# Optimization experiments

Measured on AMD Instinct MI355X. Metric: run time of the kernel, lower is better.

Reference implementation:

```python
import jax, jax.numpy as jnp
import numpy as np

N_HEADS = 4
DIM_K = 64
DIM_V = 64
D_MODEL = 256


def setup_inputs() -> dict:
    key = jax.random.key(0)
    ks = jax.random.split(key, 10)
    B, S = 8, 1024
    s = 1.0 / np.sqrt(D_MODEL)
    return {
        "x": jax.random.normal(ks[0], (B, S, D_MODEL), jnp.float32),
        "y": jax.random.normal(ks[1], (B, S, D_MODEL), jnp.float32),
        "Wq": jax.random.normal(ks[2], (D_MODEL, DIM_K * N_HEADS), jnp.float32) * s,
        "bq": jnp.zeros((DIM_K * N_HEADS,), jnp.float32),
        "Wk": jax.random.normal(ks[3], (D_MODEL, DIM_K * N_HEADS), jnp.float32) * s,
        "bk": jnp.zeros((DIM_K * N_HEADS,), jnp.float32),
        "Wv": jax.random.normal(ks[4], (D_MODEL, DIM_V * N_HEADS), jnp.float32) * s,
        "bv": jnp.zeros((DIM_V * N_HEADS,), jnp.float32),
        "Wo": jax.random.normal(ks[5], (DIM_V * N_HEADS, D_MODEL), jnp.float32) * s,
        "bo": jnp.zeros((D_MODEL,), jnp.float32),
    }


def reference(x, y, Wq, bq, Wk, bk, Wv, bv, Wo, bo):
    B, Sx, _ = x.shape
    Sy = y.shape[1]
    dk = DIM_K // N_HEADS  # head dim for Q/K (16)
    dv = DIM_V // N_HEADS  # head dim for V (16)
    # Faithful to the original reshape: leading dim becomes n_heads^2 pseudo-heads.
    Q = (x @ Wq + bq).reshape(-1, B, Sx, dk)   # [H2, B, Sx, dk]
    K = (y @ Wk + bk).reshape(-1, B, Sy, dk)   # [H2, B, Sy, dk]
    V = (y @ Wv + bv).reshape(-1, B, Sy, dv)   # [H2, B, Sy, dv]
    scale = 1.0 / np.sqrt(DIM_K)
    scores = jnp.einsum("hbqd,hbkd->hbqk", Q, K) * scale  # [H2, B, Sx, Sy]
    # Per-row lower median (torch.median semantics: lower of two middle values).
    n = scores.shape[-1]
    med = jnp.sort(scores, axis=-1)[..., (n - 1) // 2][..., None]
    # Mask out entries not strictly greater than the row median.
    scores = jnp.where(scores - med > 0, scores, -jnp.inf)
    probs = jax.nn.softmax(scores, axis=-1)
    out = jnp.einsum("hbqk,hbkd->hbqd", probs, V)          # [H2, B, Sx, dv]
    out = jnp.transpose(out, (0, 2, 1, 3)).reshape(B, Sx, -1)  # [B, Sx, H2*dv]
    return out @ Wo + bo
```

## Files before the change

### kernel.cpp

```cpp
#include <hip/hip_runtime.h>
#include <stdint.h>


typedef _Float16 f16x8 __attribute__((ext_vector_type(8)));
typedef _Float16 f16x4 __attribute__((ext_vector_type(4)));
typedef _Float16 f16x2 __attribute__((ext_vector_type(2)));
typedef float    f32x4 __attribute__((ext_vector_type(4)));

__device__ __forceinline__ void gemm_mfma(const float* __restrict__ A,
                                          const float* __restrict__ W,
                                          const float* __restrict__ bias,
                                          float* __restrict__ C)
{
    __shared__ _Float16 Bhi[64][136];
    __shared__ _Float16 Blo[64][136];
    const int tid = threadIdx.x;
    const int m0 = blockIdx.x << 6, n0 = blockIdx.y << 6;

    const int wv = tid >> 6, lane = tid & 63;
    const int fm = lane & 15, fq = lane >> 4;
    const int arow = m0 + (wv << 4) + fm;

    f32x4 acc[4];
    #pragma unroll
    for (int cb = 0; cb < 4; ++cb) { acc[cb][0]=0.f; acc[cb][1]=0.f; acc[cb][2]=0.f; acc[cb][3]=0.f; }

    #pragma unroll
    for (int h = 0; h < 2; ++h) {
        if (h) __syncthreads();
        {
            const int kk = (tid & 63) << 1;
            const int nh = (tid >> 6) << 4;
            const float* w0 = W + (size_t)((h << 7) + kk) * 256 + n0 + nh;
            const float* w1 = w0 + 256;
            #pragma unroll
            for (int c4 = 0; c4 < 4; ++c4) {
                float4 v0 = *(const float4*)(w0 + (c4 << 2));
                float4 v1 = *(const float4*)(w1 + (c4 << 2));
                const float e0[4] = {v0.x, v0.y, v0.z, v0.w};
                const float e1[4] = {v1.x, v1.y, v1.z, v1.w};
                #pragma unroll
                for (int jj = 0; jj < 4; ++jj) {
                    const int n = nh + (c4 << 2) + jj;
                    _Float16 h0 = (_Float16)e0[jj];
                    _Float16 h1 = (_Float16)e1[jj];
                    f16x2 hp; hp[0] = h0; hp[1] = h1;
                    f16x2 lp; lp[0] = (_Float16)(e0[jj] - (float)h0);
                              lp[1] = (_Float16)(e1[jj] - (float)h1);
                    *(f16x2*)&Bhi[n][kk] = hp;
                    *(f16x2*)&Blo[n][kk] = lp;
                }
            }
        }
        __syncthreads();

        #pragma unroll
        for (int kb = 0; kb < 4; ++kb) {
            const float* ap = A + (size_t)arow * 256 + (h << 7) + (kb << 5) + (fq << 3);
            float4 a0 = *(const float4*)ap;
            float4 a1 = *(const float4*)(ap + 4);
            const float ae[8] = {a0.x, a0.y, a0.z, a0.w, a1.x, a1.y, a1.z, a1.w};
            f16x8 Ah, Al;
            #pragma unroll
            for (int j = 0; j < 8; ++j) {
                _Float16 hh = (_Float16)ae[j];
                Ah[j] = hh;
                Al[j] = (_Float16)(ae[j] - (float)hh);
            }
            #pragma unroll
            for (int cb = 0; cb < 4; ++cb) {
                f16x8 Bh = *(const f16x8*)&Bhi[(cb << 4) + fm][(kb << 5) + (fq << 3)];
                f16x8 Bl = *(const f16x8*)&Blo[(cb << 4) + fm][(kb << 5) + (fq << 3)];
                acc[cb] = __builtin_amdgcn_mfma_f32_16x16x32_f16(Ah, Bh, acc[cb], 0, 0, 0);
                acc[cb] = __builtin_amdgcn_mfma_f32_16x16x32_f16(Al, Bh, acc[cb], 0, 0, 0);
                acc[cb] = __builtin_amdgcn_mfma_f32_16x16x32_f16(Ah, Bl, acc[cb], 0, 0, 0);
            }
        }
    }

    #pragma unroll
    for (int cb = 0; cb < 4; ++cb) {
        const float bb = bias[n0 + (cb << 4) + fm];
        #pragma unroll
        for (int i = 0; i < 4; ++i)
            C[(size_t)(m0 + (wv << 4) + (fq << 2) + i) * 256
              + n0 + (cb << 4) + fm] = acc[cb][i] + bb;
    }
}

__global__ __attribute__((amdgpu_waves_per_eu(4, 4)))
__launch_bounds__(256) void gemmQKV(
    const float* __restrict__ x, const float* __restrict__ y,
    const float* __restrict__ Wq, const float* __restrict__ bq,
    const float* __restrict__ Wk, const float* __restrict__ bk,
    const float* __restrict__ Wv, const float* __restrict__ bv,
    float* __restrict__ Q, float* __restrict__ K, float* __restrict__ V)
{
    const int z = blockIdx.z;
    const float* A = (z == 0) ? x  : y;
    const float* W = (z == 0) ? Wq : (z == 1) ? Wk : Wv;
    const float* b = (z == 0) ? bq : (z == 1) ? bk : bv;
    float*       C = (z == 0) ? Q  : (z == 1) ? K  : V;
    gemm_mfma(A, W, b, C);
}

__global__ __attribute__((amdgpu_waves_per_eu(4, 4)))
__launch_bounds__(256) void gemmOut(
    const float* __restrict__ A, const float* __restrict__ W,
    const float* __restrict__ b, float* __restrict__ C)
{
    gemm_mfma(A, W, b, C);
}

__device__ __forceinline__ float u2f(unsigned int m) {
    unsigned int x = (m & 0x80000000u) ? (m ^ 0x80000000u) : ~m;
    return __uint_as_float(x);
}
__device__ __forceinline__ unsigned int f2u(float f) {
    unsigned int x = __float_as_uint(f);
    return (x & 0x80000000u) ? ~x : (x | 0x80000000u);
}

__device__ __forceinline__ float wred_sum(float x) {
    x += __int_as_float(__builtin_amdgcn_update_dpp(0, __float_as_int(x), 0x111, 0xF, 0xF, true));
    x += __int_as_float(__builtin_amdgcn_update_dpp(0, __float_as_int(x), 0x112, 0xF, 0xF, true));
    x += __int_as_float(__builtin_amdgcn_update_dpp(0, __float_as_int(x), 0x114, 0xF, 0xF, true));
    x += __int_as_float(__builtin_amdgcn_update_dpp(0, __float_as_int(x), 0x118, 0xF, 0xF, true));
    x += __int_as_float(__builtin_amdgcn_update_dpp(0, __float_as_int(x), 0x142, 0xF, 0xF, true));
    x += __int_as_float(__builtin_amdgcn_update_dpp(0, __float_as_int(x), 0x143, 0xF, 0xF, true));
    return __int_as_float(__builtin_amdgcn_readlane(__float_as_int(x), 63));
}
__device__ __forceinline__ float wred_min(float x) {
    const int IDENT = 0x7f7fffff;
    x = fminf(x, __int_as_float(__builtin_amdgcn_update_dpp(IDENT, __float_as_int(x), 0x111, 0xF, 0xF, false)));
    x = fminf(x, __int_as_float(__builtin_amdgcn_update_dpp(IDENT, __float_as_int(x), 0x112, 0xF, 0xF, false)));
    x = fminf(x, __int_as_float(__builtin_amdgcn_update_dpp(IDENT, __float_as_int(x), 0x114, 0xF, 0xF, false)));
    x = fminf(x, __int_as_float(__builtin_amdgcn_update_dpp(IDENT, __float_as_int(x), 0x118, 0xF, 0xF, false)));
    x = fminf(x, __int_as_float(__builtin_amdgcn_update_dpp(IDENT, __float_as_int(x), 0x142, 0xF, 0xF, false)));
    x = fminf(x, __int_as_float(__builtin_amdgcn_update_dpp(IDENT, __float_as_int(x), 0x143, 0xF, 0xF, false)));
    return __int_as_float(__builtin_amdgcn_readlane(__float_as_int(x), 63));
}
__device__ __forceinline__ float wred_max(float x) {
    const int IDENT = (int)0xff7fffff;
    x = fmaxf(x, __int_as_float(__builtin_amdgcn_update_dpp(IDENT, __float_as_int(x), 0x111, 0xF, 0xF, false)));
    x = fmaxf(x, __int_as_float(__builtin_amdgcn_update_dpp(IDENT, __float_as_int(x), 0x112, 0xF, 0xF, false)));
    x = fmaxf(x, __int_as_float(__builtin_amdgcn_update_dpp(IDENT, __float_as_int(x), 0x114, 0xF, 0xF, false)));
    x = fmaxf(x, __int_as_float(__builtin_amdgcn_update_dpp(IDENT, __float_as_int(x), 0x118, 0xF, 0xF, false)));
    x = fmaxf(x, __int_as_float(__builtin_amdgcn_update_dpp(IDENT, __float_as_int(x), 0x142, 0xF, 0xF, false)));
    x = fmaxf(x, __int_as_float(__builtin_amdgcn_update_dpp(IDENT, __float_as_int(x), 0x143, 0xF, 0xF, false)));
    return __int_as_float(__builtin_amdgcn_readlane(__float_as_int(x), 63));
}

__global__ __attribute__((amdgpu_waves_per_eu(6, 6)))
__launch_bounds__(512) void attn(
    const float* __restrict__ Qb, const float* __restrict__ Kb,
    const float* __restrict__ Vb, float* __restrict__ Ob)
{
    __shared__ union {
        float    Ssc[8][1028];
        _Float16 Vt[16][1032];
    } U;
    __shared__ float part[1024];
    __shared__ float sums[2][8];

    const int tid  = threadIdx.x;
    const int wave = tid >> 6, lane = tid & 63;
    const int head = blockIdx.x, grp = blockIdx.y;
    const float* Qh = Qb + ((size_t)head << 14);
    const float* Kh = Kb + ((size_t)head << 14);
    const float* Vh = Vb + ((size_t)head << 14);
    const int fm = lane & 15, fq = lane >> 4;

    for (int i = tid; i < 4096; i += 512) {
        float4 v = ((const float4*)Vh)[i];
        const int k = i >> 2, d0 = (i & 3) << 2;
        U.Vt[d0 + 0][k] = (_Float16)v.x;
        U.Vt[d0 + 1][k] = (_Float16)v.y;
        U.Vt[d0 + 2][k] = (_Float16)v.z;
        U.Vt[d0 + 3][k] = (_Float16)v.w;
    }
    __syncthreads();
    f16x8 Vf[4];
    #pragma unroll
    for (int kb = 0; kb < 4; ++kb)
        Vf[kb] = *(const f16x8*)&U.Vt[fm][(((wave << 2) + kb) << 5) + (fq << 3)];

    f16x8 Bp[8];
    #pragma unroll
    for (int kb = 0; kb < 8; ++kb) {
        const int krow = (wave << 7) + (kb << 4) + fm;
        float4 kv = *(const float4*)(Kh + ((size_t)krow << 4) + (fq << 2));
        const float ke[4] = {kv.x * 0.125f, kv.y * 0.125f,
                             kv.z * 0.125f, kv.w * 0.125f};
        #pragma unroll
        for (int j = 0; j < 4; ++j) {
            _Float16 h = (_Float16)ke[j];
            Bp[kb][j]     = h;
            Bp[kb][j + 4] = (_Float16)(ke[j] - (float)h);
        }
    }
    __syncthreads();

    const int cstart = (grp * 128) / 6;
    const int cend   = ((grp + 1) * 128) / 6;

    for (int chunk = cstart; chunk < cend; ++chunk) {
        const int qbase = chunk << 3;
        const int sb = chunk & 1;

        f16x8 A1, A2;
        {
            const int arow = qbase + (fm & 7);
            float4 qv = *(const float4*)(Qh + ((size_t)arow << 4) + (fq << 2));
            const float qe[4] = {qv.x, qv.y, qv.z, qv.w};
            #pragma unroll
            for (int j = 0; j < 4; ++j) {
                _Float16 h = (_Float16)qe[j];
                A1[j] = h; A1[j + 4] = h;
                A2[j] = (_Float16)(qe[j] - (float)h);
                A2[j + 4] = (_Float16)0.f;
            }
        }
        #pragma unroll
        for (int kb = 0; kb < 8; ++kb) {
            f32x4 c = {0.f, 0.f, 0.f, 0.f};
            c = __builtin_amdgcn_mfma_f32_16x16x32_f16(A1, Bp[kb], c, 0, 0, 0);
            c = __builtin_amdgcn_mfma_f32_16x16x32_f16(A2, Bp[kb], c, 0, 0, 0);
            if (fq < 2) {
                const int col = (wave << 7) + (kb << 4) + fm;
                #pragma unroll
                for (int i = 0; i < 4; ++i)
                    U.Ssc[(fq << 2) + i][col] = c[i];
            }
        }
        __syncthreads();

        float s[16];
        #pragma unroll
        for (int b = 0; b < 4; ++b) {
            f32x4 v = *(const f32x4*)&U.Ssc[wave][(b << 8) + (lane << 2)];
            s[(b << 2) + 0] = v.x; s[(b << 2) + 1] = v.y;
            s[(b << 2) + 2] = v.z; s[(b << 2) + 3] = v.w;
        }

        float mn = 0.f, sq = 0.f;
        #pragma unroll
        for (int j = 0; j < 16; ++j) { mn += s[j]; sq += s[j] * s[j]; }
        mn = wred_sum(mn);
        sq = wred_sum(sq);
        mn *= (1.0f / 1024.0f);
        const float var  = fmaxf(sq * (1.0f / 1024.0f) - mn * mn, 1e-12f);
        const float step = __builtin_sqrtf(var) * 0.0024479f;

        unsigned int lo = 0x00800000u, hi = 0xFF7FFFFFu;
        int cl = 0, ch = 1024;
        float vL = -3.4e38f, vH = 3.4e38f;
        float t = mn, medf = 0.f;
        int found = 0;
        for (int pass = 0; pass < 64 && !found; ++pass) {
            int cnt = 0;
            #pragma unroll
            for (int j = 0; j < 16; ++j)
                cnt += __popcll(__ballot(s[j] <= t));
            const unsigned int tc = f2u(t);
            if (cnt >= 512) { hi = tc; ch = cnt; vH = t; }
            else            { lo = tc + 1; cl = cnt; vL = t; }

            if (cl == 511) {
                float c = 3.4e38f;
                #pragma unroll
                for (int j = 0; j < 16; ++j)
                    c = fminf(c, (s[j] > vL) ? s[j] : 3.4e38f);
                medf = wred_min(c); found = 1;
            } else if (ch == 512) {
                float c = -3.4e38f;
                #pragma unroll
                for (int j = 0; j < 16; ++j)
                    c = fmaxf(c, (s[j] <= vH) ? s[j] : -3.4e38f);
                medf = wred_max(c); found = 1;
            } else if (cl == 510) {
                float m1 = 3.4e38f;
                #pragma unroll
                for (int j = 0; j < 16; ++j)
                    m1 = fminf(m1, (s[j] > vL) ? s[j] : 3.4e38f);
                m1 = wred_min(m1);
                int c1 = 0;
                #pragma unroll
                for (int j = 0; j < 16; ++j)
                    c1 += __popcll(__ballot(s[j] <= m1));
                if (c1 >= 512) { medf = m1; }
                else {
                    float c2 = 3.4e38f;
                    #pragma unroll
                    for (int j = 0; j < 16; ++j)
                        c2 = fminf(c2, (s[j] > m1) ? s[j] : 3.4e38f);
                    medf = wred_min(c2);
                }
                found = 1;
            } else if (ch == 513) {
                float m1 = -3.4e38f;
                #pragma unroll
                for (int j = 0; j < 16; ++j)
                    m1 = fmaxf(m1, (s[j] <= vH) ? s[j] : -3.4e38f);
                m1 = wred_max(m1);
                int c1 = 0;
                #pragma unroll
                for (int j = 0; j < 16; ++j)
                    c1 += __popcll(__ballot(s[j] < m1));
                if (c1 <= 511) { medf = m1; }
                else {
                    float c2 = -3.4e38f;
                    #pragma unroll
                    for (int j = 0; j < 16; ++j)
                        c2 = fmaxf(c2, (s[j] < m1) ? s[j] : -3.4e38f);
                    medf = wred_max(c2);
                }
                found = 1;
            } else if (lo >= hi) {
                medf = u2f(lo); found = 1;
            } else {
                float tn = t + (511.5f - (float)cnt) * step;
                bool ok = (tn > vL) && (tn < vH);
                if (pass >= 5 && (pass & 1)) ok = false;
                t = ok ? tn : u2f(lo + ((hi - lo) >> 1));
            }
        }
        if (!found) medf = u2f(lo);

        _Float16* Pw = (_Float16*)&U.Ssc[wave][0];
        float sum = 0.f;
        #pragma unroll
        for (int b = 0; b < 4; ++b) {
            f16x4 hv;
            #pragma unroll
            for (int jj = 0; jj < 4; ++jj) {
                float e = (s[(b << 2) + jj] > medf) ? __expf(s[(b << 2) + jj]) : 0.f;
                _Float16 h = (_Float16)e;
                hv[jj] = h;
                sum += (float)h;
            }
            *(f16x4*)&Pw[(b << 8) + (lane << 2)] = hv;
        }
        sum = wred_sum(sum);
        if (lane == 0) sums[sb][wave] = sum;
        __syncthreads();

        f32x4 acc = {0.f, 0.f, 0.f, 0.f};
        const _Float16* Pr = (const _Float16*)&U.Ssc[fm & 7][0] + (fq << 3);
        #pragma unroll
        for (int kb = 0; kb < 4; ++kb) {
            f16x8 a = *(const f16x8*)(Pr + ((((wave << 2) + kb)) << 5));
            acc = __builtin_amdgcn_mfma_f32_16x16x32_f16(a, Vf[kb], acc, 0, 0, 0);
        }
        if (lane < 32) {
            #pragma unroll
            for (int i = 0; i < 4; ++i)
                part[(wave << 7) + (((fq << 2) + i) << 4) + fm] = acc[i];
        }
        __syncthreads();

        const int rw = (wave - chunk) & 7;
        if (rw < 2) {
            const int t2 = (rw << 6) + lane;
            const int r = t2 >> 4, d = t2 & 15;
            float o = 0.f;
            #pragma unroll
            for (int w = 0; w < 8; ++w) o += part[(w << 7) + t2];
            const float inv = 1.0f / sums[sb][r];
            const int q = qbase + r;
            const int h = head >> 3, bp = head & 7;
            float* dst = Ob + (((size_t)(h >> 1)) << 18)
                            + ((size_t)(((h & 1) << 9) + (q >> 1)) << 8)
                            + ((q & 1) << 7) + (bp << 4) + d;
            *dst = o * inv;
        }
    }
}

extern "C" void kernel_launch(void* const* d_in, const int* in_sizes, int n_in,
                              void* d_out, int out_size, void* d_ws, size_t ws_size,
                              hipStream_t stream) {
    const float* x  = (const float*)d_in[0];
    const float* y  = (const float*)d_in[1];
    const float* Wq = (const float*)d_in[2];
    const float* bq = (const float*)d_in[3];
    const float* Wk = (const float*)d_in[4];
    const float* bk = (const float*)d_in[5];
    const float* Wv = (const float*)d_in[6];
    const float* bv = (const float*)d_in[7];
    const float* Wo = (const float*)d_in[8];
    const float* bo = (const float*)d_in[9];
    float* out = (float*)d_out;

    float* Q  = (float*)d_ws;
    float* K  = Q + 2097152;
    float* V  = K + 2097152;
    float* AO = V + 2097152;

    gemmQKV<<<dim3(128, 4, 3), dim3(256), 0, stream>>>(x, y, Wq, bq, Wk, bk,
                                                       Wv, bv, Q, K, V);
    attn<<<dim3(128, 6), dim3(512), 0, stream>>>(Q, K, V, AO);
    gemmOut<<<dim3(128, 4), dim3(256), 0, stream>>>(AO, Wo, bo, out);
}
```

Before: 285.1 us.

## Use secant-based median search and prefetch A/Q operands one step ahead

Changes the median search to a secant step built from the previous threshold and count, falling back to the fixed step otherwise, and delays the forced bisection from pass 5 to pass 8. The goal is fewer ballot-count passes per row. Also prefetches the next A tile in the projection GEMM and the next Q row in the attention loop so load latency overlaps compute, and splits the min/max reductions into two accumulators to shorten dependency chains. The prefetches keep extra values live in registers, and the secant step could take more passes on some rows.

```diff
diff --git a/kernel.cpp b/kernel.cpp
--- a/kernel.cpp
+++ b/kernel.cpp
@@ -20,10 +20,14 @@
     const int wv = tid >> 6, lane = tid & 63;
     const int fm = lane & 15, fq = lane >> 4;
     const int arow = m0 + (wv << 4) + fm;
+    const float* abase = A + (size_t)arow * 256;
 
     f32x4 acc[4];
     #pragma unroll
     for (int cb = 0; cb < 4; ++cb) { acc[cb][0]=0.f; acc[cb][1]=0.f; acc[cb][2]=0.f; acc[cb][3]=0.f; }
+
+    float4 a0 = *(const float4*)(abase + (fq << 3));
+    float4 a1 = *(const float4*)(abase + (fq << 3) + 4);
 
     #pragma unroll
     for (int h = 0; h < 2; ++h) {
@@ -56,9 +60,13 @@
 
         #pragma unroll
         for (int kb = 0; kb < 4; ++kb) {
-            const float* ap = A + (size_t)arow * 256 + (h << 7) + (kb << 5) + (fq << 3);
-            float4 a0 = *(const float4*)ap;
-            float4 a1 = *(const float4*)(ap + 4);
+            const int ks = (h << 2) + kb;
+            float4 n0v = a0, n1v = a1;
+            if (ks < 7) {
+                const float* np = abase + ((ks + 1) << 5) + (fq << 3);
+                n0v = *(const float4*)np;
+                n1v = *(const float4*)(np + 4);
+            }
             const float ae[8] = {a0.x, a0.y, a0.z, a0.w, a1.x, a1.y, a1.z, a1.w};
             f16x8 Ah, Al;
             #pragma unroll
@@ -75,6 +83,7 @@
                 acc[cb] = __builtin_amdgcn_mfma_f32_16x16x32_f16(Al, Bh, acc[cb], 0, 0, 0);
                 acc[cb] = __builtin_amdgcn_mfma_f32_16x16x32_f16(Ah, Bl, acc[cb], 0, 0, 0);
             }
+            a0 = n0v; a1 = n1v;
         }
     }
 
@@ -204,14 +213,18 @@
     const int cstart = (grp * 128) / 6;
     const int cend   = ((grp + 1) * 128) / 6;
 
+    float4 qv;
+    {
+        const int arow0 = (cstart << 3) + (fm & 7);
+        qv = *(const float4*)(Qh + ((size_t)arow0 << 4) + (fq << 2));
+    }
+
     for (int chunk = cstart; chunk < cend; ++chunk) {
         const int qbase = chunk << 3;
         const int sb = chunk & 1;
 
         f16x8 A1, A2;
         {
-            const int arow = qbase + (fm & 7);
-            float4 qv = *(const float4*)(Qh + ((size_t)arow << 4) + (fq << 2));
             const float qe[4] = {qv.x, qv.y, qv.z, qv.w};
             #pragma unroll
             for (int j = 0; j < 4; ++j) {
@@ -220,6 +233,10 @@
                 A2[j] = (_Float16)(qe[j] - (float)h);
                 A2[j + 4] = (_Float16)0.f;
             }
+        }
+        if (chunk + 1 < cend) {
+            const int arow = ((chunk + 1) << 3) + (fm & 7);
+            qv = *(const float4*)(Qh + ((size_t)arow << 4) + (fq << 2));
         }
         #pragma unroll
         for (int kb = 0; kb < 8; ++kb) {
@@ -256,6 +273,7 @@
         int cl = 0, ch = 1024;
         float vL = -3.4e38f, vH = 3.4e38f;
         float t = mn, medf = 0.f;
+        float tp = 0.f; int cp = -1;
         int found = 0;
         for (int pass = 0; pass < 64 && !found; ++pass) {
             int cnt = 0;
@@ -267,61 +285,83 @@
             else            { lo = tc + 1; cl = cnt; vL = t; }
 
             if (cl == 511) {
-                float c = 3.4e38f;
-                #pragma unroll
-                for (int j = 0; j < 16; ++j)
-                    c = fminf(c, (s[j] > vL) ? s[j] : 3.4e38f);
-                medf = wred_min(c); found = 1;
+                float c0 = 3.4e38f, c1 = 3.4e38f;
+                #pragma unroll
+                for (int j = 0; j < 8; ++j) {
+                    c0 = fminf(c0, (s[j]     > vL) ? s[j]     : 3.4e38f);
+                    c1 = fminf(c1, (s[j + 8] > vL) ? s[j + 8] : 3.4e38f);
+                }
+                medf = wred_min(fminf(c0, c1)); found = 1;
             } else if (ch == 512) {
-                float c = -3.4e38f;
-                #pragma unroll
-                for (int j = 0; j < 16; ++j)
-                    c = fmaxf(c, (s[j] <= vH) ? s[j] : -3.4e38f);
-                medf = wred_max(c); found = 1;
+                float c0 = -3.4e38f, c1 = -3.4e38f;
+                #pragma unroll
+                for (int j = 0; j < 8; ++j) {
+                    c0 = fmaxf(c0, (s[j]     <= vH) ? s[j]     : -3.4e38f);
+                    c1 = fmaxf(c1, (s[j + 8] <= vH) ? s[j + 8] : -3.4e38f);
+                }
+                medf = wred_max(fmaxf(c0, c1)); found = 1;
             } else if (cl == 510) {
-                float m1 = 3.4e38f;
-                #pragma unroll
-                for (int j = 0; j < 16; ++j)
-                    m1 = fminf(m1, (s[j] > vL) ? s[j] : 3.4e38f);
-                m1 = wred_min(m1);
+                float m0 = 3.4e38f, m1 = 3.4e38f;
+                #pragma unroll
+                for (int j = 0; j < 8; ++j) {
+                    m0 = fminf(m0, (s[j]     > vL) ? s[j]     : 3.4e38f);
+                    m1 = fminf(m1, (s[j + 8] > vL) ? s[j + 8] : 3.4e38f);
+                }
+                m1 = wred_min(fminf(m0, m1));
                 int c1 = 0;
                 #pragma unroll
                 for (int j = 0; j < 16; ++j)
                     c1 += __popcll(__ballot(s[j] <= m1));
                 if (c1 >= 512) { medf = m1; }
                 else {
-                    float c2 = 3.4e38f;
+                    float d0 = 3.4e38f, d1 = 3.4e38f;
                     #pragma unroll
-                    for (int j = 0; j < 16; ++j)
-                        c2 = fminf(c2, (s[j] > m1) ? s[j] : 3.4e38f);
-                    medf = wred_min(c2);
+                    for (int j = 0; j < 8; ++j) {
+                        d0 = fminf(d0, (s[j]     > m1) ? s[j]     : 3.4e38f);
+                        d1 = fminf(d1, (s[j + 8] > m1) ? s[j + 8] : 3.4e38f);
+                    }
+                    medf = wred_min(fminf(d0, d1));
                 }
                 found = 1;
             } else if (ch == 513) {
-                float m1 = -3.4e38f;
-                #pragma unroll
-                for (int j = 0; j < 16; ++j)
-                    m1 = fmaxf(m1, (s[j] <= vH) ? s[j] : -3.4e38f);
-                m1 = wred_max(m1);
+                float m0 = -3.4e38f, m1 = -3.4e38f;
+                #pragma unroll
+                for (int j = 0; j < 8; ++j) {
+                    m0 = fmaxf(m0, (s[j]     <= vH) ? s[j]     : -3.4e38f);
+                    m1 = fmaxf(m1, (s[j + 8] <= vH) ? s[j + 8] : -3.4e38f);
+                }
+                m1 = wred_max(fmaxf(m0, m1));
                 int c1 = 0;
                 #pragma unroll
                 for (int j = 0; j < 16; ++j)
                     c1 += __popcll(__ballot(s[j] < m1));
                 if (c1 <= 511) { medf = m1; }
                 else {
-                    float c2 = -3.4e38f;
+                    float d0 = -3.4e38f, d1 = -3.4e38f;
                     #pragma unroll
-                    for (int j = 0; j < 16; ++j)
-                        c2 = fmaxf(c2, (s[j] < m1) ? s[j] : -3.4e38f);
-                    medf = wred_max(c2);
+                    for (int j = 0; j < 8; ++j) {
+                        d0 = fmaxf(d0, (s[j]     < m1) ? s[j]     : -3.4e38f);
+                        d1 = fmaxf(d1, (s[j + 8] < m1) ? s[j + 8] : -3.4e38f);
+                    }
+                    medf = wred_max(fmaxf(d0, d1));
                 }
                 found = 1;
             } else if (lo >= hi) {
                 medf = u2f(lo); found = 1;
             } else {
-                float tn = t + (511.5f - (float)cnt) * step;
+                float tn;
+                bool have = false;
+                if (cp >= 0 && cnt != cp) {
+                    const float slope = (t - tp) / (float)(cnt - cp);
+                    if (slope > 0.f) {
+                        tn = t + (511.5f - (float)cnt) * slope;
+                        have = true;
+                    }
+                }
+                if (!have) tn = t + (511.5f - (float)cnt) * step;
+                tp = t; cp = cnt;
                 bool ok = (tn > vL) && (tn < vH);
-                if (pass >= 5 && (pass & 1)) ok = false;
+                if (pass >= 8 && (pass & 1)) ok = false;
                 t = ok ? tn : u2f(lo + ((hi - lo) >> 1));
             }
         }
```

Measured after the change: 305.7 us. 7.2% more time.

## Pre-split weights into fp16 hi/lo once and store V as fp16

Applied to the files above, without the earlier changes.

Adds a prepW kernel that transposes each weight matrix and splits it into fp16 high and low parts a single time. The GEMMs then read these directly from global memory instead of converting the fp32 weights in every block through LDS with syncthreads. The QKV GEMM also writes V as fp16, which halves V traffic and removes the conversion in the attention kernel. The cost is one extra kernel launch, more workspace, and GEMM B-operand reads that now come from global or L2 without LDS staging.

```diff
diff --git a/kernel.cpp b/kernel.cpp
--- a/kernel.cpp
+++ b/kernel.cpp
@@ -4,112 +4,128 @@
 
 typedef _Float16 f16x8 __attribute__((ext_vector_type(8)));
 typedef _Float16 f16x4 __attribute__((ext_vector_type(4)));
-typedef _Float16 f16x2 __attribute__((ext_vector_type(2)));
 typedef float    f32x4 __attribute__((ext_vector_type(4)));
 
+__global__ __launch_bounds__(256) void prepW(
+    const float* __restrict__ Wq, const float* __restrict__ Wk,
+    const float* __restrict__ Wv, const float* __restrict__ Wo,
+    _Float16* __restrict__ P)
+{
+    __shared__ float T[64][65];
+    const int mat = blockIdx.y;
+    const float* W = (mat == 0) ? Wq : (mat == 1) ? Wk : (mat == 2) ? Wv : Wo;
+    const int tk = blockIdx.x >> 2, tn = blockIdx.x & 3;
+    const int t  = threadIdx.x;
+    const int cl = t & 63, rg = t >> 6;
+
+    #pragma unroll
+    for (int r = 0; r < 16; ++r) {
+        const int k = (rg << 4) + r;
+        T[k][cl] = W[(size_t)((tk << 6) + k) * 256 + (tn << 6) + cl];
+    }
+    __syncthreads();
+    _Float16* hi = P + ((size_t)mat << 17);
+    _Float16* lo = hi + 65536;
+    #pragma unroll
+    for (int r = 0; r < 16; ++r) {
+        const int n = (rg << 4) + r;
+        const float v = T[cl][n];
+        const _Float16 h = (_Float16)v;
+        const size_t o = (size_t)((tn << 6) + n) * 256 + (tk << 6) + cl;
+        hi[o] = h;
+        lo[o] = (_Float16)(v - (float)h);
+    }
+}
+
 __device__ __forceinline__ void gemm_mfma(const float* __restrict__ A,
-                                          const float* __restrict__ W,
+                                          const _Float16* __restrict__ Whi,
+                                          const _Float16* __restrict__ Wlo,
                                           const float* __restrict__ bias,
-                                          float* __restrict__ C)
+                                          float* __restrict__ C, int vf16)
 {
-    __shared__ _Float16 Bhi[64][136];
-    __shared__ _Float16 Blo[64][136];
     const int tid = threadIdx.x;
     const int m0 = blockIdx.x << 6, n0 = blockIdx.y << 6;
-
     const int wv = tid >> 6, lane = tid & 63;
     const int fm = lane & 15, fq = lane >> 4;
     const int arow = m0 + (wv << 4) + fm;
+    const float*     abase = A   + (size_t)arow * 256 + (fq << 3);
+    const _Float16*  bh0   = Whi + (size_t)(n0 + fm) * 256 + (fq << 3);
+    const _Float16*  bl0   = Wlo + (size_t)(n0 + fm) * 256 + (fq << 3);
 
     f32x4 acc[4];
     #pragma unroll
     for (int cb = 0; cb < 4; ++cb) { acc[cb][0]=0.f; acc[cb][1]=0.f; acc[cb][2]=0.f; acc[cb][3]=0.f; }
 
-    #pragma unroll
-    for (int h = 0; h < 2; ++h) {
-        if (h) __syncthreads();
-        {
-            const int kk = (tid & 63) << 1;
-            const int nh = (tid >> 6) << 4;
-            const float* w0 = W + (size_t)((h << 7) + kk) * 256 + n0 + nh;
-            const float* w1 = w0 + 256;
-            #pragma unroll
-            for (int c4 = 0; c4 < 4; ++c4) {
-                float4 v0 = *(const float4*)(w0 + (c4 << 2));
-                float4 v1 = *(const float4*)(w1 + (c4 << 2));
-                const float e0[4] = {v0.x, v0.y, v0.z, v0.w};
-                const float e1[4] = {v1.x, v1.y, v1.z, v1.w};
-                #pragma unroll
-                for (int jj = 0; jj < 4; ++jj) {
-                    const int n = nh + (c4 << 2) + jj;
-                    _Float16 h0 = (_Float16)e0[jj];
-                    _Float16 h1 = (_Float16)e1[jj];
-                    f16x2 hp; hp[0] = h0; hp[1] = h1;
-                    f16x2 lp; lp[0] = (_Float16)(e0[jj] - (float)h0);
-                              lp[1] = (_Float16)(e1[jj] - (float)h1);
-                    *(f16x2*)&Bhi[n][kk] = hp;
-                    *(f16x2*)&Blo[n][kk] = lp;
-                }
-            }
-        }
-        __syncthreads();
-
-        #pragma unroll
-        for (int kb = 0; kb < 4; ++kb) {
-            const float* ap = A + (size_t)arow * 256 + (h << 7) + (kb << 5) + (fq << 3);
-            float4 a0 = *(const float4*)ap;
-            float4 a1 = *(const float4*)(ap + 4);
-            const float ae[8] = {a0.x, a0.y, a0.z, a0.w, a1.x, a1.y, a1.z, a1.w};
-            f16x8 Ah, Al;
-            #pragma unroll
-            for (int j = 0; j < 8; ++j) {
-                _Float16 hh = (_Float16)ae[j];
-                Ah[j] = hh;
-                Al[j] = (_Float16)(ae[j] - (float)hh);
-            }
-            #pragma unroll
-            for (int cb = 0; cb < 4; ++cb) {
-                f16x8 Bh = *(const f16x8*)&Bhi[(cb << 4) + fm][(kb << 5) + (fq << 3)];
-                f16x8 Bl = *(const f16x8*)&Blo[(cb << 4) + fm][(kb << 5) + (fq << 3)];
-                acc[cb] = __builtin_amdgcn_mfma_f32_16x16x32_f16(Ah, Bh, acc[cb], 0, 0, 0);
-                acc[cb] = __builtin_amdgcn_mfma_f32_16x16x32_f16(Al, Bh, acc[cb], 0, 0, 0);
-                acc[cb] = __builtin_amdgcn_mfma_f32_16x16x32_f16(Ah, Bl, acc[cb], 0, 0, 0);
-            }
-        }
-    }
-
-    #pragma unroll
-    for (int cb = 0; cb < 4; ++cb) {
-        const float bb = bias[n0 + (cb << 4) + fm];
-        #pragma unroll
-        for (int i = 0; i < 4; ++i)
-            C[(size_t)(m0 + (wv << 4) + (fq << 2) + i) * 256
-              + n0 + (cb << 4) + fm] = acc[cb][i] + bb;
+    #pragma unroll 2
+    for (int ks = 0; ks < 8; ++ks) {
+        float4 a0 = *(const float4*)(abase + (ks << 5));
+        float4 a1 = *(const float4*)(abase + (ks << 5) + 4);
+        const float ae[8] = {a0.x, a0.y, a0.z, a0.w, a1.x, a1.y, a1.z, a1.w};
+        f16x8 Ah, Al;
+        #pragma unroll
+        for (int j = 0; j < 8; ++j) {
+            const _Float16 hh = (_Float16)ae[j];
+            Ah[j] = hh;
+            Al[j] = (_Float16)(ae[j] - (float)hh);
+        }
+        #pragma unroll
+        for (int cb = 0; cb < 4; ++cb) {
+            const size_t off = ((size_t)(cb << 4) << 8) + (ks << 5);
+            f16x8 Bh = *(const f16x8*)(bh0 + off);
+            f16x8 Bl = *(const f16x8*)(bl0 + off);
+            acc[cb] = __builtin_amdgcn_mfma_f32_16x16x32_f16(Ah, Bh, acc[cb], 0, 0, 0);
+            acc[cb] = __builtin_amdgcn_mfma_f32_16x16x32_f16(Al, Bh, acc[cb], 0, 0, 0);
+            acc[cb] = __builtin_amdgcn_mfma_f32_16x16x32_f16(Ah, Bl, acc[cb], 0, 0, 0);
+        }
+    }
+
+    if (vf16) {
+        _Float16* Cv = (_Float16*)C;
+        #pragma unroll
+        for (int cb = 0; cb < 4; ++cb) {
+            const float bb = bias[n0 + (cb << 4) + fm];
+            #pragma unroll
+            for (int i = 0; i < 4; ++i)
+                Cv[(size_t)(m0 + (wv << 4) + (fq << 2) + i) * 256
+                   + n0 + (cb << 4) + fm] = (_Float16)(acc[cb][i] + bb);
+        }
+    } else {
+        #pragma unroll
+        for (int cb = 0; cb < 4; ++cb) {
+            const float bb = bias[n0 + (cb << 4) + fm];
+            #pragma unroll
+            for (int i = 0; i < 4; ++i)
+                C[(size_t)(m0 + (wv << 4) + (fq << 2) + i) * 256
+                  + n0 + (cb << 4) + fm] = acc[cb][i] + bb;
+        }
     }
 }
 
 __global__ __attribute__((amdgpu_waves_per_eu(4, 4)))
 __launch_bounds__(256) void gemmQKV(
     const float* __restrict__ x, const float* __restrict__ y,
-    const float* __restrict__ Wq, const float* __restrict__ bq,
-    const float* __restrict__ Wk, const float* __restrict__ bk,
-    const float* __restrict__ Wv, const float* __restrict__ bv,
-    float* __restrict__ Q, float* __restrict__ K, float* __restrict__ V)
+    const _Float16* __restrict__ WP,
+    const float* __restrict__ bq, const float* __restrict__ bk,
+    const float* __restrict__ bv,
+    float* __restrict__ Q, float* __restrict__ K, float* __restrict__ Vf)
 {
     const int z = blockIdx.z;
     const float* A = (z == 0) ? x  : y;
-    const float* W = (z == 0) ? Wq : (z == 1) ? Wk : Wv;
+    const _Float16* Whi = WP + ((size_t)z << 17);
+    const _Float16* Wlo = Whi + 65536;
     const float* b = (z == 0) ? bq : (z == 1) ? bk : bv;
-    float*       C = (z == 0) ? Q  : (z == 1) ? K  : V;
-    gemm_mfma(A, W, b, C);
+    float*       C = (z == 0) ? Q  : (z == 1) ? K  : Vf;
+    gemm_mfma(A, Whi, Wlo, b, C, z == 2);
 }
 
 __global__ __attribute__((amdgpu_waves_per_eu(4, 4)))
 __launch_bounds__(256) void gemmOut(
-    const float* __restrict__ A, const float* __restrict__ W,
+    const float* __restrict__ A, const _Float16* __restrict__ WP,
     const float* __restrict__ b, float* __restrict__ C)
 {
-    gemm_mfma(A, W, b, C);
+    const _Float16* Whi = WP + ((size_t)3 << 17);
+    const _Float16* Wlo = Whi + 65536;
+    gemm_mfma(A, Whi, Wlo, b, C, 0);
 }
 
 __device__ __forceinline__ float u2f(unsigned int m) {
@@ -154,7 +170,7 @@
 __global__ __attribute__((amdgpu_waves_per_eu(6, 6)))
 __launch_bounds__(512) void attn(
     const float* __restrict__ Qb, const float* __restrict__ Kb,
-    const float* __restrict__ Vb, float* __restrict__ Ob)
+    const _Float16* __restrict__ Vb, float* __restrict__ Ob)
 {
     __shared__ union {
         float    Ssc[8][1028];
@@ -166,18 +182,18 @@
     const int tid  = threadIdx.x;
     const int wave = tid >> 6, lane = tid & 63;
     const int head = blockIdx.x, grp = blockIdx.y;
-    const float* Qh = Qb + ((size_t)head << 14);
-    const float* Kh = Kb + ((size_t)head << 14);
-    const float* Vh = Vb + ((size_t)head << 14);
+    const float*    Qh = Qb + ((size_t)head << 14);
+    const float*    Kh = Kb + ((size_t)head << 14);
+    const _Float16* Vh = Vb + ((size_t)head << 14);
     const int fm = lane & 15, fq = lane >> 4;
 
     for (int i = tid; i < 4096; i += 512) {
-        float4 v = ((const float4*)Vh)[i];
+        f16x4 v = ((const f16x4*)Vh)[i];
         const int k = i >> 2, d0 = (i & 3) << 2;
-        U.Vt[d0 + 0][k] = (_Float16)v.x;
-        U.Vt[d0 + 1][k] = (_Float16)v.y;
-        U.Vt[d0 + 2][k] = (_Float16)v.z;
-        U.Vt[d0 + 3][k] = (_Float16)v.w;
+        U.Vt[d0 + 0][k] = v[0];
+        U.Vt[d0 + 1][k] = v[1];
+        U.Vt[d0 + 2][k] = v[2];
+        U.Vt[d0 + 3][k] = v[3];
     }
     __syncthreads();
     f16x8 Vf[4];
@@ -392,13 +408,15 @@
     const float* bo = (const float*)d_in[9];
     float* out = (float*)d_out;
 
-    float* Q  = (float*)d_ws;
-    float* K  = Q + 2097152;
-    float* V  = K + 2097152;
-    float* AO = V + 2097152;
-
-    gemmQKV<<<dim3(128, 4, 3), dim3(256), 0, stream>>>(x, y, Wq, bq, Wk, bk,
-                                                       Wv, bv, Q, K, V);
+    float*     Q  = (float*)d_ws;
+    float*     K  = Q + 2097152;
+    _Float16*  V  = (_Float16*)(K + 2097152);
+    float*     AO = (float*)d_ws + 5242880;
+    _Float16*  WP = (_Float16*)((float*)d_ws + 7340032);
+
+    prepW<<<dim3(16, 4), dim3(256), 0, stream>>>(Wq, Wk, Wv, Wo, WP);
+    gemmQKV<<<dim3(128, 4, 3), dim3(256), 0, stream>>>(x, y, WP, bq, bk, bv,
+                                                       Q, K, (float*)V);
     attn<<<dim3(128, 6), dim3(512), 0, stream>>>(Q, K, V, AO);
-    gemmOut<<<dim3(128, 4), dim3(256), 0, stream>>>(AO, Wo, bo, out);
-}
+    gemmOut<<<dim3(128, 4), dim3(256), 0, stream>>>(AO, WP, bo, out);
+}
```

New measurement: 321.2 us. 1.13x slower.
